# Kernel tuning notes

Measured on AMD Instinct MI355X. Metric: run time of the kernel, lower is better.

Reference implementation:

```python
import jax, jax.numpy as jnp
import numpy as np

B, S, H = 4, 2048, 2048
N_HEADS, KV_HEADS, RANK = 16, 8, 64
HEAD_DIM = H // N_HEADS          # 128
N_REP = N_HEADS // KV_HEADS      # 2
NEG = -1e9


def setup_inputs() -> dict:
    key = jax.random.key(0)
    ks = jax.random.split(key, 6)
    hidden_states = jax.random.normal(ks[0], (B, S, H), dtype=jnp.float32)
    # additive causal mask, broadcast over heads: [B,1,S,S]
    causal = jnp.tril(jnp.ones((S, S), dtype=bool))
    attention_mask = jnp.where(causal, 0.0, NEG).astype(jnp.float32)
    attention_mask = jnp.broadcast_to(attention_mask[None, None], (B, 1, S, S))
    sc = 1.0 / np.sqrt(H)
    Wq = jax.random.normal(ks[1], (H, RANK), dtype=jnp.float32) * sc
    Wk = jax.random.normal(ks[2], (H, RANK), dtype=jnp.float32) * sc
    Wv = jax.random.normal(ks[3], (H, KV_HEADS * HEAD_DIM), dtype=jnp.float32) * sc
    Wo = jax.random.normal(ks[4], (H, H), dtype=jnp.float32) * sc
    return {"hidden_states": hidden_states, "attention_mask": attention_mask,
            "Wq": Wq, "Wk": Wk, "Wv": Wv, "Wo": Wo}


def reference(hidden_states, attention_mask, Wq, Wk, Wv, Wo):
    b, s, h = hidden_states.shape
    # low-rank CP factors shared across heads: [B,S,R]
    q = hidden_states @ Wq
    k = hidden_states @ Wk
    # values with GQA: [B, kv_heads, S, head_dim] -> repeat to [B, n_heads, S, head_dim]
    v = (hidden_states @ Wv).reshape(b, s, KV_HEADS, HEAD_DIM).transpose(0, 2, 1, 3)
    v = jnp.repeat(v, N_REP, axis=1)
    # CP circuit over the (i,j) grid: scores[b,i,j] = sum_r q[b,i,r] * k[b,j,r]
    # (Hadamard over embedding factors gathered at grid indices, SumLayer with unit
    #  weights over rank; the all-ones head factor multiplies by 1). Head-shared.
    scores = jnp.einsum('bir,bjr->bij', q, k)[:, None]  # [B,1,S,S]
    scores = scores + attention_mask                     # additive causal mask
    probs = jax.nn.softmax(scores.astype(jnp.float32), axis=-1).astype(v.dtype)
    # attn_probs @ V, broadcasting the head-shared probs over heads
    ctx = jnp.einsum('bij,bhjd->bhid', probs[:, 0], v)   # [B,H,S,D]
    ctx = ctx.transpose(0, 2, 1, 3).reshape(b, s, h)
    return ctx @ Wo
```

## Files before the change

kernel.cpp:

```cpp
#include <hip/hip_runtime.h>

#define B_ 4
#define S_ 2048
#define H_ 2048
#define R_ 64
#define DKV_ 1024

typedef __attribute__((ext_vector_type(8))) short s16x8;
typedef __attribute__((ext_vector_type(4))) float f32x4v;

__device__ __forceinline__ unsigned short f2bf(float x) {
  unsigned int u = __builtin_bit_cast(unsigned int, x);
  u += 0x7FFF + ((u >> 16) & 1);
  return (unsigned short)(u >> 16);
}
__device__ __forceinline__ float bf2f(unsigned short h) {
  unsigned int u = ((unsigned int)h) << 16;
  return __builtin_bit_cast(float, u);
}

__device__ __forceinline__ void gl_lds16(const void* g, void* l) {
  __builtin_amdgcn_global_load_lds(
      (const __attribute__((address_space(1))) unsigned int*)g,
      (__attribute__((address_space(3))) unsigned int*)l, 16, 0, 0);
}

__device__ __forceinline__ int swz_off(int m, int kb) {
  int L = m >> 1;
  int slot = ((m & 1) << 2) | (kb >> 4);
  int sp = slot ^ (L & 7);
  return (L << 7) | (sp << 4) | (kb & 15);
}

__global__ __launch_bounds__(256) void k_f32_to_bf16x2(const float* __restrict__ in,
    unsigned short* __restrict__ hi, unsigned short* __restrict__ lo, int n4) {
  int i = blockIdx.x * 256 + threadIdx.x;
  if (i >= n4) return;
  float4 v = ((const float4*)in)[i];
  ushort4 h, l;
  h.x = f2bf(v.x); h.y = f2bf(v.y); h.z = f2bf(v.z); h.w = f2bf(v.w);
  l.x = f2bf(v.x - bf2f(h.x)); l.y = f2bf(v.y - bf2f(h.y));
  l.z = f2bf(v.z - bf2f(h.z)); l.w = f2bf(v.w - bf2f(h.w));
  ((ushort4*)hi)[i] = h;
  ((ushort4*)lo)[i] = l;
}

__global__ __launch_bounds__(256) void k_transpose_bf16(const float* __restrict__ in,
    unsigned short* __restrict__ out, int rows, int cols) {
  __shared__ float tile[32][33];
  int c0 = blockIdx.x * 32, r0 = blockIdx.y * 32;
  int tx = threadIdx.x & 31, ty = threadIdx.x >> 5;
  for (int i = 0; i < 4; ++i)
    tile[ty + i * 8][tx] = in[(size_t)(r0 + ty + i * 8) * cols + c0 + tx];
  __syncthreads();
  for (int i = 0; i < 4; ++i)
    out[(size_t)(c0 + ty + i * 8) * rows + r0 + tx] = f2bf(tile[tx][ty + i * 8]);
}

__global__ __launch_bounds__(256) void k_build_wqkt(const float* __restrict__ Wq,
    const float* __restrict__ Wk, unsigned short* __restrict__ hiT,
    unsigned short* __restrict__ loT) {
  __shared__ float tile[32][33];
  int k0 = blockIdx.x * 32, n0 = blockIdx.y * 32;
  const float* W = (n0 < 64) ? Wq : Wk;
  int nb = n0 & 63;
  int tx = threadIdx.x & 31, ty = threadIdx.x >> 5;
  for (int i = 0; i < 4; ++i)
    tile[ty + i * 8][tx] = W[(size_t)(k0 + ty + i * 8) * R_ + nb + tx];
  __syncthreads();
  for (int i = 0; i < 4; ++i) {
    float v = tile[tx][ty + i * 8];
    unsigned short h = f2bf(v);
    size_t idx = (size_t)(n0 + ty + i * 8) * H_ + k0 + tx;
    hiT[idx] = h;
    loT[idx] = f2bf(v - bf2f(h));
  }
}

__global__ __launch_bounds__(256) void k_build_wot(const float* __restrict__ Wo,
                                                   unsigned short* __restrict__ WoT) {
  __shared__ float tile[32][33];
  int n0 = blockIdx.x * 32, r0 = blockIdx.y * 32;
  int h1b = 256 * (r0 >> 7) + (r0 & 127);
  int tx = threadIdx.x & 31, ty = threadIdx.x >> 5;
  for (int i = 0; i < 4; ++i) {
    int dr = ty + i * 8;
    tile[dr][tx] = Wo[(size_t)(h1b + dr) * H_ + n0 + tx] +
                   Wo[(size_t)(h1b + 128 + dr) * H_ + n0 + tx];
  }
  __syncthreads();
  for (int i = 0; i < 4; ++i)
    WoT[(size_t)(n0 + ty + i * 8) * DKV_ + r0 + tx] = f2bf(tile[tx][ty + i * 8]);
}

__global__ __launch_bounds__(256) void k_qk_mfma(
    const unsigned short* __restrict__ Ahi, const unsigned short* __restrict__ Alo,
    const unsigned short* __restrict__ Bhi, const unsigned short* __restrict__ Blo,
    unsigned short* __restrict__ qkh, unsigned short* __restrict__ qkl) {
  constexpr int TQK = 20480;
  __shared__ __attribute__((aligned(16))) char lds[3 * TQK];
  int m0 = blockIdx.x * 32;
  int t = threadIdx.x;
  int lane = t & 63, wave = t >> 6;
  int lr = lane & 15, kb = (lane >> 4) << 4;

  auto stage = [&](int kt, int buf) {
    int k0 = kt << 5;
    char* base = &lds[buf * TQK];
    {
      int q = t & 127;
      int L = q >> 3;
      int slot = (q & 7) ^ (L & 7);
      int m = (L << 1) | (slot >> 2);
      int ke = (slot & 3) << 3;
      const unsigned short* src =
          (t < 128 ? Ahi : Alo) + (size_t)(m0 + m) * H_ + k0 + ke;
      gl_lds16(src, base + (t < 128 ? 0 : 2048) + q * 16);
    }
#pragma unroll
    for (int c = 0; c < 2; ++c) {
      int q = c * 256 + t;
      int L = q >> 3;
      int slot = (q & 7) ^ (L & 7);
      int n = (L << 1) | (slot >> 2);
      int ke = (slot & 3) << 3;
      gl_lds16(Bhi + (size_t)n * H_ + k0 + ke, base + 4096 + q * 16);
    }
#pragma unroll
    for (int c = 0; c < 2; ++c) {
      int q = c * 256 + t;
      int L = q >> 3;
      int slot = (q & 7) ^ (L & 7);
      int n = (L << 1) | (slot >> 2);
      int ke = (slot & 3) << 3;
      gl_lds16(Blo + (size_t)n * H_ + k0 + ke, base + 12288 + q * 16);
    }
  };

  f32x4v acc[2][2] = {};
  stage(0, 0);
  stage(1, 1);
  int cur = 0, nxt = 2;
  for (int kt = 0; kt < 64; ++kt) {
    __builtin_amdgcn_sched_barrier(0);
    if (kt < 63) asm volatile("s_waitcnt vmcnt(5)" ::: "memory");
    else asm volatile("s_waitcnt vmcnt(0)" ::: "memory");
    __builtin_amdgcn_s_barrier();
    __builtin_amdgcn_sched_barrier(0);
    if (kt + 2 < 64) stage(kt + 2, nxt);
    const char* base = &lds[cur * TQK];
    s16x8 ah[2], al[2], bh[2], bl[2];
#pragma unroll
    for (int m = 0; m < 2; ++m) {
      int o = swz_off(m * 16 + lr, kb);
      ah[m] = *(const s16x8*)(base + o);
      al[m] = *(const s16x8*)(base + 2048 + o);
    }
#pragma unroll
    for (int n = 0; n < 2; ++n) {
      int o = swz_off(wave * 32 + n * 16 + lr, kb);
      bh[n] = *(const s16x8*)(base + 4096 + o);
      bl[n] = *(const s16x8*)(base + 12288 + o);
    }
    __builtin_amdgcn_s_setprio(1);
#pragma unroll
    for (int m = 0; m < 2; ++m)
#pragma unroll
      for (int n = 0; n < 2; ++n) {
        acc[m][n] = __builtin_amdgcn_mfma_f32_16x16x32_bf16(ah[m], bh[n], acc[m][n], 0, 0, 0);
        acc[m][n] = __builtin_amdgcn_mfma_f32_16x16x32_bf16(ah[m], bl[n], acc[m][n], 0, 0, 0);
        acc[m][n] = __builtin_amdgcn_mfma_f32_16x16x32_bf16(al[m], bh[n], acc[m][n], 0, 0, 0);
      }
    __builtin_amdgcn_s_setprio(0);
    cur = (cur == 2) ? 0 : cur + 1;
    nxt = (nxt == 2) ? 0 : nxt + 1;
  }
  for (int m = 0; m < 2; ++m) {
    int lrow = m * 16 + ((lane >> 4) << 2);
    for (int n = 0; n < 2; ++n) {
      int lcol = wave * 32 + n * 16 + lr;
      for (int r = 0; r < 4; ++r) {
        float v = acc[m][n][r];
        unsigned short h = f2bf(v);
        size_t idx = (size_t)(m0 + lrow + r) * 128 + lcol;
        qkh[idx] = h;
        qkl[idx] = f2bf(v - bf2f(h));
      }
    }
  }
}

__global__ __launch_bounds__(256) void k_scores_mfma(
    const unsigned short* __restrict__ qkh, const unsigned short* __restrict__ qkl,
    unsigned short* __restrict__ probs, float* __restrict__ part) {
  __shared__ unsigned short AsH[128 * 32], AsL[128 * 32];
  __shared__ unsigned short BsH[128 * 32], BsL[128 * 32];
  __shared__ float psum[128];
  int tri = blockIdx.x, b = blockIdx.y;
  int t = threadIdx.x;
  int it = (int)((sqrtf(8.f * tri + 1.f) - 1.f) * 0.5f);
  while ((it + 1) * (it + 2) / 2 <= tri) ++it;
  while (it * (it + 1) / 2 > tri) --it;
  int jt = tri - it * (it + 1) / 2;
  int i0 = it * 128, j0 = jt * 128;
  const unsigned short* Ah = qkh + (size_t)(b * S_ + i0) * 128;
  const unsigned short* Al = qkl + (size_t)(b * S_ + i0) * 128;
  const unsigned short* Bh = qkh + (size_t)(b * S_ + j0) * 128 + 64;
  const unsigned short* Bl = qkl + (size_t)(b * S_ + j0) * 128 + 64;
  if (t < 128) psum[t] = 0.f;
  int lane = t & 63, wave = t >> 6;
  int wr = wave >> 1, wc = wave & 1;
  int lr = lane & 15, lk = (lane >> 4) * 8;
  f32x4v acc[4][4] = {};
  for (int k0 = 0; k0 < 64; k0 += 32) {
    for (int c = 0; c < 2; ++c) {
      int id = c * 256 + t;
      int row = id >> 2, kc = (id & 3) * 8;
      gl_lds16(Ah + (size_t)row * 128 + k0 + kc, &AsH[row * 32 + kc]);
      gl_lds16(Al + (size_t)row * 128 + k0 + kc, &AsL[row * 32 + kc]);
      gl_lds16(Bh + (size_t)row * 128 + k0 + kc, &BsH[row * 32 + kc]);
      gl_lds16(Bl + (size_t)row * 128 + k0 + kc, &BsL[row * 32 + kc]);
    }
    __syncthreads();
    s16x8 ah[4], al[4], bh[4], bl[4];
    for (int m = 0; m < 4; ++m) {
      ah[m] = *(const s16x8*)&AsH[(wr * 64 + m * 16 + lr) * 32 + lk];
      al[m] = *(const s16x8*)&AsL[(wr * 64 + m * 16 + lr) * 32 + lk];
    }
    for (int n = 0; n < 4; ++n) {
      bh[n] = *(const s16x8*)&BsH[(wc * 64 + n * 16 + lr) * 32 + lk];
      bl[n] = *(const s16x8*)&BsL[(wc * 64 + n * 16 + lr) * 32 + lk];
    }
    for (int m = 0; m < 4; ++m)
      for (int n = 0; n < 4; ++n) {
        acc[m][n] = __builtin_amdgcn_mfma_f32_16x16x32_bf16(ah[m], bh[n], acc[m][n], 0, 0, 0);
        acc[m][n] = __builtin_amdgcn_mfma_f32_16x16x32_bf16(ah[m], bl[n], acc[m][n], 0, 0, 0);
        acc[m][n] = __builtin_amdgcn_mfma_f32_16x16x32_bf16(al[m], bh[n], acc[m][n], 0, 0, 0);
      }
    __syncthreads();
  }
  unsigned short* Pp = probs + (size_t)b * S_ * S_;
  for (int m = 0; m < 4; ++m) {
    int lrow = wr * 64 + m * 16 + ((lane >> 4) << 2);
    float ps[4] = {0.f, 0.f, 0.f, 0.f};
    for (int n = 0; n < 4; ++n) {
      int j = j0 + wc * 64 + n * 16 + lr;
      for (int r = 0; r < 4; ++r) {
        int i = i0 + lrow + r;
        float p = (j <= i) ? __expf(acc[m][n][r]) : 0.f;
        ps[r] += p;
        Pp[(size_t)i * S_ + j] = f2bf(p);
      }
    }
    for (int r = 0; r < 4; ++r) {
      float v = ps[r];
      for (int msk = 1; msk < 16; msk <<= 1) v += __shfl_xor(v, msk, 64);
      if (lr == 0) atomicAdd(&psum[lrow + r], v);
    }
  }
  __syncthreads();
  if (t < 128) part[(size_t)(b * 16 + jt) * S_ + i0 + t] = psum[t];
}

__global__ __launch_bounds__(256) void k_rowsum_recip(const float* __restrict__ part,
                                                      float* __restrict__ recip) {
  int g = blockIdx.x * 256 + threadIdx.x;
  int b = g >> 11, i = g & (S_ - 1);
  int it = i >> 7;
  float s = 0.f;
  for (int jt = 0; jt <= it; ++jt) s += part[(size_t)(b * 16 + jt) * S_ + i];
  recip[(size_t)b * S_ + i] = 1.f / s;
}

template <int BM, int BN, bool TRANS_OUT, bool OUT_BF16, bool SCALE, bool CAUSAL>
__global__ __launch_bounds__(512, 4) void k_gemm256(
    const unsigned short* __restrict__ A, int lda, long batchA,
    const unsigned short* __restrict__ BT, int ldbt, long batchBT,
    void* __restrict__ C, int ldc, long batchC,
    const float* __restrict__ recip, int batchR, int K) {
  constexpr int ABYTES = BM * 64;
  constexpr int BBYTES = BN * 64;
  constexpr int TILEB = ABYTES + BBYTES;
  constexpr int WARPS_M = (BM >= 256) ? 4 : 2;
  constexpr int WARPS_N = 8 / WARPS_M;
  constexpr int WM = BM / WARPS_M;
  constexpr int WN = BN / WARPS_N;
  constexpr int MF = WM / 16;
  constexpr int NF = WN / 16;
  constexpr int LPS = BM / 128 + BN / 128;
  __shared__ __attribute__((aligned(16))) char lds[3 * TILEB];
  __shared__ float s_recip[BM];

  int t = threadIdx.x;
  int gx = gridDim.x;
  int bx, by;
  if (CAUSAL) {
    int x = blockIdx.x;
    bx = (x & 1) ? (gx - 1 - (x >> 1)) : (x >> 1);
    if (blockIdx.z & 2) bx = gx - 1 - bx;
    by = blockIdx.y;
  } else {
    int id = blockIdx.y * gx + blockIdx.x;
    int cpx = gx >> 3;
    int xcd = id & 7, rr = id >> 3;
    bx = xcd * cpx + rr % cpx;
    by = rr / cpx;
  }
  int z = blockIdx.z;
  int m0 = bx * BM, n0 = by * BN;

  const unsigned short* Ab = A + (long)z * batchA + (size_t)m0 * lda;
  const unsigned short* Bb = BT + (long)z * batchBT + (size_t)n0 * ldbt;

  if (SCALE && t < BM) s_recip[t] = recip[(long)z * batchR + m0 + t];

  int lane = t & 63, wave = t >> 6;
  int wr = wave / WARPS_N, wc = wave % WARPS_N;
  int kb = (lane >> 4) << 4;
  int aoff[MF], boff[NF];
#pragma unroll
  for (int mf = 0; mf < MF; ++mf)
    aoff[mf] = swz_off(wr * WM + mf * 16 + (lane & 15), kb);
#pragma unroll
  for (int nf = 0; nf < NF; ++nf)
    boff[nf] = swz_off(wc * WN + nf * 16 + (lane & 15), kb);

  int NT = (CAUSAL ? (m0 + BM) : K) >> 5;

  auto stage = [&](int kt, int buf) {
    int k0 = kt << 5;
    char* la = &lds[buf * TILEB];
    char* lb = la + ABYTES;
#pragma unroll
    for (int c = 0; c < BM / 128; ++c) {
      int q = c * 512 + t;
      int L = q >> 3;
      int slot = (q & 7) ^ (L & 7);
      int m = (L << 1) | (slot >> 2);
      int ke = (slot & 3) << 3;
      gl_lds16(Ab + (size_t)m * lda + k0 + ke, la + q * 16);
    }
#pragma unroll
    for (int c = 0; c < BN / 128; ++c) {
      int q = c * 512 + t;
      int L = q >> 3;
      int slot = (q & 7) ^ (L & 7);
      int n = (L << 1) | (slot >> 2);
      int ke = (slot & 3) << 3;
      gl_lds16(Bb + (size_t)n * ldbt + k0 + ke, lb + q * 16);
    }
  };

  f32x4v acc[MF][NF] = {};
  stage(0, 0);
  if (NT > 1) stage(1, 1);
  int cur = 0, nxt = 2;
  for (int kt = 0; kt < NT; ++kt) {
    __builtin_amdgcn_sched_barrier(0);
    if (kt + 1 < NT) {
      if constexpr (LPS == 2) asm volatile("s_waitcnt vmcnt(2)" ::: "memory");
      else if constexpr (LPS == 3) asm volatile("s_waitcnt vmcnt(3)" ::: "memory");
      else asm volatile("s_waitcnt vmcnt(4)" ::: "memory");
    } else {
      asm volatile("s_waitcnt vmcnt(0)" ::: "memory");
    }
    __builtin_amdgcn_s_barrier();
    __builtin_amdgcn_sched_barrier(0);
    if (kt + 2 < NT) stage(kt + 2, nxt);
    const char* la = &lds[cur * TILEB];
    const char* lb = la + ABYTES;
    s16x8 af[MF], bf[NF];
#pragma unroll
    for (int mf = 0; mf < MF; ++mf) af[mf] = *(const s16x8*)(la + aoff[mf]);
#pragma unroll
    for (int nf = 0; nf < NF; ++nf) bf[nf] = *(const s16x8*)(lb + boff[nf]);
    __builtin_amdgcn_s_setprio(1);
#pragma unroll
    for (int mf = 0; mf < MF; ++mf)
#pragma unroll
      for (int nf = 0; nf < NF; ++nf)
        acc[mf][nf] =
            __builtin_amdgcn_mfma_f32_16x16x32_bf16(af[mf], bf[nf], acc[mf][nf], 0, 0, 0);
    __builtin_amdgcn_s_setprio(0);
    cur = (cur == 2) ? 0 : cur + 1;
    nxt = (nxt == 2) ? 0 : nxt + 1;
  }

#pragma unroll
  for (int mf = 0; mf < MF; ++mf) {
    int lrow = wr * WM + mf * 16 + ((lane >> 4) << 2);
#pragma unroll
    for (int nf = 0; nf < NF; ++nf) {
      int lcol = wc * WN + nf * 16 + (lane & 15);
      f32x4v v = acc[mf][nf];
      if (TRANS_OUT) {
        float f0 = v[0], f1 = v[1], f2 = v[2], f3 = v[3];
        if (SCALE) {
          f0 *= s_recip[lrow]; f1 *= s_recip[lrow + 1];
          f2 *= s_recip[lrow + 2]; f3 *= s_recip[lrow + 3];
        }
        ushort4 o;
        o.x = f2bf(f0); o.y = f2bf(f1); o.z = f2bf(f2); o.w = f2bf(f3);
        unsigned short* Cp = (unsigned short*)C + (long)z * batchC;
        *(ushort4*)&Cp[(size_t)(n0 + lcol) * ldc + m0 + lrow] = o;
      } else {
#pragma unroll
        for (int r = 0; r < 4; ++r) {
          float f = v[r];
          if (SCALE) f *= s_recip[lrow + r];
          if (OUT_BF16) {
            unsigned short* Cp = (unsigned short*)C + (long)z * batchC;
            Cp[(size_t)(m0 + lrow + r) * ldc + n0 + lcol] = f2bf(f);
          } else {
            float* Cp = (float*)C + (long)z * batchC;
            Cp[(size_t)(m0 + lrow + r) * ldc + n0 + lcol] = f;
          }
        }
      }
    }
  }
}

extern "C" void kernel_launch(void* const* d_in, const int* in_sizes, int n_in,
                              void* d_out, int out_size, void* d_ws, size_t ws_size,
                              hipStream_t stream) {
  const float* hs = (const float*)d_in[0];
  const float* Wq = (const float*)d_in[2];
  const float* Wk = (const float*)d_in[3];
  const float* Wv = (const float*)d_in[4];
  const float* Wo = (const float*)d_in[5];
  float* out = (float*)d_out;

  char* w = (char*)d_ws;
  unsigned short* hsb = (unsigned short*)w; w += (size_t)B_ * S_ * H_ * 2;
  unsigned short* hsl = (unsigned short*)w; w += (size_t)B_ * S_ * H_ * 2;
  unsigned short* WvT = (unsigned short*)w; w += (size_t)DKV_ * H_ * 2;
  unsigned short* WoT = (unsigned short*)w; w += (size_t)H_ * DKV_ * 2;
  unsigned short* WqkTh = (unsigned short*)w; w += (size_t)128 * H_ * 2;
  unsigned short* WqkTl = (unsigned short*)w; w += (size_t)128 * H_ * 2;
  unsigned short* VT  = (unsigned short*)w; w += (size_t)DKV_ * B_ * S_ * 2;
  unsigned short* probs = (unsigned short*)w; w += (size_t)B_ * S_ * S_ * 2;
  unsigned short* ctx = (unsigned short*)w; w += (size_t)B_ * S_ * DKV_ * 2;
  unsigned short* qkh = (unsigned short*)w; w += (size_t)B_ * S_ * 128 * 2;
  unsigned short* qkl = (unsigned short*)w; w += (size_t)B_ * S_ * 128 * 2;
  float* part = (float*)w; w += (size_t)B_ * 16 * S_ * 4;
  float* recip = (float*)w; w += (size_t)B_ * S_ * 4;

  k_f32_to_bf16x2<<<(B_ * S_ * H_ / 4 + 255) / 256, 256, 0, stream>>>(
      hs, hsb, hsl, B_ * S_ * H_ / 4);
  k_transpose_bf16<<<dim3(DKV_ / 32, H_ / 32), 256, 0, stream>>>(Wv, WvT, H_, DKV_);
  k_build_wot<<<dim3(H_ / 32, DKV_ / 32), 256, 0, stream>>>(Wo, WoT);
  k_build_wqkt<<<dim3(H_ / 32, 4), 256, 0, stream>>>(Wq, Wk, WqkTh, WqkTl);
  k_qk_mfma<<<B_ * S_ / 32, 256, 0, stream>>>(hsb, hsl, WqkTh, WqkTl, qkh, qkl);
  k_gemm256<256, 128, true, true, false, false>
      <<<dim3(B_ * S_ / 256, DKV_ / 128, 1), 512, 0, stream>>>(
      hsb, H_, 0, WvT, H_, 0, VT, B_ * S_, 0, nullptr, 0, H_);
  k_scores_mfma<<<dim3(136, B_), 256, 0, stream>>>(qkh, qkl, probs, part);
  k_rowsum_recip<<<B_ * S_ / 256, 256, 0, stream>>>(part, recip);
  k_gemm256<128, 128, false, true, true, true>
      <<<dim3(S_ / 128, DKV_ / 128, B_), 512, 0, stream>>>(
      probs, S_, (long)S_ * S_, VT, B_ * S_, S_, ctx, DKV_, (long)S_ * DKV_, recip, S_, S_);
  k_gemm256<256, 128, false, false, false, false>
      <<<dim3(B_ * S_ / 256, H_ / 128, 1), 512, 0, stream>>>(
      ctx, DKV_, 0, WoT, DKV_, 0, out, H_, 0, nullptr, 0, DKV_);
}
```

Baseline: 211.0 us.

## Split GEMM k-loop into two half-MFMA phases interleaved with staged loads

Splits each k-iteration of the bf16 GEMM into two phases. Each phase loads half the A fragments from LDS, issues either the A or the B global-to-LDS prefetch for tile kt+2, then runs half the MFMAs, with extra barriers and lgkmcnt waits between phases. The aim is to spread the memory issue across the compute and interleave LDS reads with MFMA work, in the style of a ping-pong schedule. The vmcnt wait is also changed to 3 for the LPS==4 configuration. The cost is two more workgroup barriers per iteration. The vmcnt accounting is a risk because the loads are now issued in split order.

New measurement: 211.5 us. No clear change (+0.2%).

```diff
diff --git a/kernel.cpp b/kernel.cpp
--- a/kernel.cpp
+++ b/kernel.cpp
@@ -287,6 +287,7 @@
   constexpr int WN = BN / WARPS_N;
   constexpr int MF = WM / 16;
   constexpr int NF = WN / 16;
+  constexpr int MH = MF / 2;
   constexpr int LPS = BM / 128 + BN / 128;
   __shared__ __attribute__((aligned(16))) char lds[3 * TILEB];
   __shared__ float s_recip[BM];
@@ -327,10 +328,9 @@
 
   int NT = (CAUSAL ? (m0 + BM) : K) >> 5;
 
-  auto stage = [&](int kt, int buf) {
+  auto stageA = [&](int kt, int buf) {
     int k0 = kt << 5;
     char* la = &lds[buf * TILEB];
-    char* lb = la + ABYTES;
 #pragma unroll
     for (int c = 0; c < BM / 128; ++c) {
       int q = c * 512 + t;
@@ -340,6 +340,10 @@
       int ke = (slot & 3) << 3;
       gl_lds16(Ab + (size_t)m * lda + k0 + ke, la + q * 16);
     }
+  };
+  auto stageB = [&](int kt, int buf) {
+    int k0 = kt << 5;
+    char* lb = &lds[buf * TILEB] + ABYTES;
 #pragma unroll
     for (int c = 0; c < BN / 128; ++c) {
       int q = c * 512 + t;
@@ -352,36 +356,56 @@
   };
 
   f32x4v acc[MF][NF] = {};
-  stage(0, 0);
-  if (NT > 1) stage(1, 1);
+  stageA(0, 0); stageB(0, 0);
+  if (NT > 1) { stageA(1, 1); stageB(1, 1); }
   int cur = 0, nxt = 2;
   for (int kt = 0; kt < NT; ++kt) {
     __builtin_amdgcn_sched_barrier(0);
     if (kt + 1 < NT) {
       if constexpr (LPS == 2) asm volatile("s_waitcnt vmcnt(2)" ::: "memory");
-      else if constexpr (LPS == 3) asm volatile("s_waitcnt vmcnt(3)" ::: "memory");
-      else asm volatile("s_waitcnt vmcnt(4)" ::: "memory");
+      else asm volatile("s_waitcnt vmcnt(3)" ::: "memory");
     } else {
       asm volatile("s_waitcnt vmcnt(0)" ::: "memory");
     }
     __builtin_amdgcn_s_barrier();
     __builtin_amdgcn_sched_barrier(0);
-    if (kt + 2 < NT) stage(kt + 2, nxt);
     const char* la = &lds[cur * TILEB];
     const char* lb = la + ABYTES;
-    s16x8 af[MF], bf[NF];
-#pragma unroll
-    for (int mf = 0; mf < MF; ++mf) af[mf] = *(const s16x8*)(la + aoff[mf]);
-#pragma unroll
-    for (int nf = 0; nf < NF; ++nf) bf[nf] = *(const s16x8*)(lb + boff[nf]);
+    s16x8 af0[MH], bfv[NF], af1[MH];
+#pragma unroll
+    for (int mf = 0; mf < MH; ++mf) af0[mf] = *(const s16x8*)(la + aoff[mf]);
+#pragma unroll
+    for (int nf = 0; nf < NF; ++nf) bfv[nf] = *(const s16x8*)(lb + boff[nf]);
+    if (kt + 2 < NT) stageA(kt + 2, nxt);
+    __builtin_amdgcn_sched_barrier(0);
+    __builtin_amdgcn_s_barrier();
+    asm volatile("s_waitcnt lgkmcnt(0)" ::: "memory");
+    __builtin_amdgcn_sched_barrier(0);
     __builtin_amdgcn_s_setprio(1);
 #pragma unroll
-    for (int mf = 0; mf < MF; ++mf)
+    for (int mf = 0; mf < MH; ++mf)
 #pragma unroll
       for (int nf = 0; nf < NF; ++nf)
         acc[mf][nf] =
-            __builtin_amdgcn_mfma_f32_16x16x32_bf16(af[mf], bf[nf], acc[mf][nf], 0, 0, 0);
+            __builtin_amdgcn_mfma_f32_16x16x32_bf16(af0[mf], bfv[nf], acc[mf][nf], 0, 0, 0);
     __builtin_amdgcn_s_setprio(0);
+    __builtin_amdgcn_sched_barrier(0);
+#pragma unroll
+    for (int mf = 0; mf < MH; ++mf) af1[mf] = *(const s16x8*)(la + aoff[MH + mf]);
+    if (kt + 2 < NT) stageB(kt + 2, nxt);
+    __builtin_amdgcn_sched_barrier(0);
+    __builtin_amdgcn_s_barrier();
+    asm volatile("s_waitcnt lgkmcnt(0)" ::: "memory");
+    __builtin_amdgcn_sched_barrier(0);
+    __builtin_amdgcn_s_setprio(1);
+#pragma unroll
+    for (int mf = 0; mf < MH; ++mf)
+#pragma unroll
+      for (int nf = 0; nf < NF; ++nf)
+        acc[MH + mf][nf] =
+            __builtin_amdgcn_mfma_f32_16x16x32_bf16(af1[mf], bfv[nf], acc[MH + mf][nf], 0, 0, 0);
+    __builtin_amdgcn_s_setprio(0);
+    __builtin_amdgcn_sched_barrier(0);
     cur = (cur == 2) ? 0 : cur + 1;
     nxt = (nxt == 2) ? 0 : nxt + 1;
   }
```

## Fuse causal scores, exp, rowsum and P@V into one attention kernel

Applied to the files above, without the earlier changes.

Replaces the separate scores kernel (which wrote a full bf16 probability matrix to global memory), the rowsum reciprocal kernel and the batched causal P@V GEMM with one fused kernel. Each block takes 64 query rows by 256 value columns, computes scores for each 32-key chunk in registers, exponentiates and masks them, stores P in LDS, and runs the P@V MFMAs. The row sums are normalised at the end. This removes the 32MB-scale probs write and read and two launches. In exchange, each d-column block recomputes the scores (4x redundant QK work), the tiles are smaller and there are two barriers per k-step.

After: 201.8 us. 4.4% less time.

```diff
diff --git a/kernel.cpp b/kernel.cpp
--- a/kernel.cpp
+++ b/kernel.cpp
@@ -190,129 +190,189 @@
   }
 }
 
-__global__ __launch_bounds__(256) void k_scores_mfma(
+__global__ __launch_bounds__(512, 4) void k_attn_fused(
     const unsigned short* __restrict__ qkh, const unsigned short* __restrict__ qkl,
-    unsigned short* __restrict__ probs, float* __restrict__ part) {
-  __shared__ unsigned short AsH[128 * 32], AsL[128 * 32];
-  __shared__ unsigned short BsH[128 * 32], BsL[128 * 32];
-  __shared__ float psum[128];
-  int tri = blockIdx.x, b = blockIdx.y;
+    const unsigned short* __restrict__ VT, unsigned short* __restrict__ ctx) {
+  constexpr int TILEB = 24576;
+  __shared__ __attribute__((aligned(16))) char lds[3 * TILEB + 4096 + 256];
+  char* Pt = &lds[3 * TILEB];
+  float* rs = (float*)&lds[3 * TILEB + 4096];
+
   int t = threadIdx.x;
-  int it = (int)((sqrtf(8.f * tri + 1.f) - 1.f) * 0.5f);
-  while ((it + 1) * (it + 2) / 2 <= tri) ++it;
-  while (it * (it + 1) / 2 > tri) --it;
-  int jt = tri - it * (it + 1) / 2;
-  int i0 = it * 128, j0 = jt * 128;
-  const unsigned short* Ah = qkh + (size_t)(b * S_ + i0) * 128;
-  const unsigned short* Al = qkl + (size_t)(b * S_ + i0) * 128;
-  const unsigned short* Bh = qkh + (size_t)(b * S_ + j0) * 128 + 64;
-  const unsigned short* Bl = qkl + (size_t)(b * S_ + j0) * 128 + 64;
-  if (t < 128) psum[t] = 0.f;
+  int gx = gridDim.x;
+  int x = blockIdx.x;
+  int bx = (x & 1) ? (gx - 1 - (x >> 1)) : (x >> 1);
+  if (blockIdx.z & 2) bx = gx - 1 - bx;
+  int z = blockIdx.z;
+  int m0 = bx * 64, d0 = blockIdx.y * 256;
+
   int lane = t & 63, wave = t >> 6;
-  int wr = wave >> 1, wc = wave & 1;
-  int lr = lane & 15, lk = (lane >> 4) * 8;
-  f32x4v acc[4][4] = {};
-  for (int k0 = 0; k0 < 64; k0 += 32) {
+  int sm = wave >> 1, sn = wave & 1;
+  int wr = wave >> 2, wc = wave & 3;
+  int kb = (lane >> 4) << 4;
+
+  const unsigned short* qh = qkh + (size_t)z * S_ * 128;
+  const unsigned short* ql = qkl + (size_t)z * S_ * 128;
+
+  s16x8 qfh[2], qfl[2];
+  {
+    size_t rq = (size_t)(m0 + sm * 16 + (lane & 15)) * 128 + ((lane >> 4) << 3);
+    qfh[0] = *(const s16x8*)(qh + rq);
+    qfh[1] = *(const s16x8*)(qh + rq + 32);
+    qfl[0] = *(const s16x8*)(ql + rq);
+    qfl[1] = *(const s16x8*)(ql + rq + 32);
+  }
+
+  auto stage = [&](int kt, int buf) {
+    int j0 = kt << 5;
+    char* base = &lds[buf * TILEB];
+    {
+      int q = t & 127;
+      int L = q >> 3;
+      int slot = (q & 7) ^ (L & 7);
+      int jr = (L << 1) | (slot >> 2);
+      int ke = (slot & 3) << 3;
+      int sub = t >> 7;
+      const unsigned short* src = ((sub < 2) ? qh : ql) +
+          (size_t)(j0 + jr) * 128 + 64 + ((sub & 1) << 5) + ke;
+      gl_lds16(src, base + sub * 2048 + q * 16);
+    }
+    char* vb = base + 8192;
+#pragma unroll
     for (int c = 0; c < 2; ++c) {
-      int id = c * 256 + t;
-      int row = id >> 2, kc = (id & 3) * 8;
-      gl_lds16(Ah + (size_t)row * 128 + k0 + kc, &AsH[row * 32 + kc]);
-      gl_lds16(Al + (size_t)row * 128 + k0 + kc, &AsL[row * 32 + kc]);
-      gl_lds16(Bh + (size_t)row * 128 + k0 + kc, &BsH[row * 32 + kc]);
-      gl_lds16(Bl + (size_t)row * 128 + k0 + kc, &BsL[row * 32 + kc]);
-    }
-    __syncthreads();
-    s16x8 ah[4], al[4], bh[4], bl[4];
-    for (int m = 0; m < 4; ++m) {
-      ah[m] = *(const s16x8*)&AsH[(wr * 64 + m * 16 + lr) * 32 + lk];
-      al[m] = *(const s16x8*)&AsL[(wr * 64 + m * 16 + lr) * 32 + lk];
-    }
-    for (int n = 0; n < 4; ++n) {
-      bh[n] = *(const s16x8*)&BsH[(wc * 64 + n * 16 + lr) * 32 + lk];
-      bl[n] = *(const s16x8*)&BsL[(wc * 64 + n * 16 + lr) * 32 + lk];
-    }
-    for (int m = 0; m < 4; ++m)
-      for (int n = 0; n < 4; ++n) {
-        acc[m][n] = __builtin_amdgcn_mfma_f32_16x16x32_bf16(ah[m], bh[n], acc[m][n], 0, 0, 0);
-        acc[m][n] = __builtin_amdgcn_mfma_f32_16x16x32_bf16(ah[m], bl[n], acc[m][n], 0, 0, 0);
-        acc[m][n] = __builtin_amdgcn_mfma_f32_16x16x32_bf16(al[m], bh[n], acc[m][n], 0, 0, 0);
+      int q = c * 512 + t;
+      int L = q >> 3;
+      int slot = (q & 7) ^ (L & 7);
+      int dr = (L << 1) | (slot >> 2);
+      int ke = (slot & 3) << 3;
+      gl_lds16(VT + (size_t)(d0 + dr) * (B_ * S_) + (size_t)z * S_ + j0 + ke,
+               vb + q * 16);
+    }
+  };
+
+  if (t < 64) rs[t] = 0.f;
+  int NT = (m0 + 64) >> 5;
+  stage(0, 0);
+  stage(1, 1);
+
+  int jrow = sn * 16 + (lane & 15);
+  int koffs = swz_off(jrow, kb);
+  int paoff[2], voff[4];
+#pragma unroll
+  for (int mf = 0; mf < 2; ++mf)
+    paoff[mf] = swz_off(wr * 32 + mf * 16 + (lane & 15), kb);
+#pragma unroll
+  for (int nf = 0; nf < 4; ++nf)
+    voff[nf] = swz_off(wc * 64 + nf * 16 + (lane & 15), kb);
+
+  float ps[4] = {0.f, 0.f, 0.f, 0.f};
+  f32x4v accp[2][4] = {};
+  int prow = sm * 16 + ((lane >> 4) << 2);
+  int pcol = sn * 16 + (lane & 15);
+
+  int cur = 0, nxt = 2;
+  for (int kt = 0; kt < NT; ++kt) {
+    __builtin_amdgcn_sched_barrier(0);
+    if (kt + 1 < NT) asm volatile("s_waitcnt vmcnt(3) lgkmcnt(0)" ::: "memory");
+    else asm volatile("s_waitcnt vmcnt(0) lgkmcnt(0)" ::: "memory");
+    __builtin_amdgcn_s_barrier();
+    __builtin_amdgcn_sched_barrier(0);
+    if (kt + 2 < NT) stage(kt + 2, nxt);
+    const char* base = &lds[cur * TILEB];
+    s16x8 kh[2], kl[2];
+    kh[0] = *(const s16x8*)(base + koffs);
+    kh[1] = *(const s16x8*)(base + 2048 + koffs);
+    kl[0] = *(const s16x8*)(base + 4096 + koffs);
+    kl[1] = *(const s16x8*)(base + 6144 + koffs);
+    f32x4v s = {};
+#pragma unroll
+    for (int ks = 0; ks < 2; ++ks) {
+      s = __builtin_amdgcn_mfma_f32_16x16x32_bf16(qfh[ks], kh[ks], s, 0, 0, 0);
+      s = __builtin_amdgcn_mfma_f32_16x16x32_bf16(qfh[ks], kl[ks], s, 0, 0, 0);
+      s = __builtin_amdgcn_mfma_f32_16x16x32_bf16(qfl[ks], kh[ks], s, 0, 0, 0);
+    }
+    int jg = (kt << 5) + pcol;
+    int ig = m0 + prow;
+#pragma unroll
+    for (int r = 0; r < 4; ++r) {
+      float p = (jg <= ig + r) ? __expf(s[r]) : 0.f;
+      ps[r] += p;
+      *(unsigned short*)(Pt + swz_off(prow + r, pcol * 2)) = f2bf(p);
+    }
+    __builtin_amdgcn_sched_barrier(0);
+    asm volatile("s_waitcnt lgkmcnt(0)" ::: "memory");
+    __builtin_amdgcn_s_barrier();
+    __builtin_amdgcn_sched_barrier(0);
+    s16x8 pa[2], vf[4];
+#pragma unroll
+    for (int mf = 0; mf < 2; ++mf) pa[mf] = *(const s16x8*)(Pt + paoff[mf]);
+    const char* vbase = base + 8192;
+#pragma unroll
+    for (int nf = 0; nf < 4; ++nf) vf[nf] = *(const s16x8*)(vbase + voff[nf]);
+    __builtin_amdgcn_s_setprio(1);
+#pragma unroll
+    for (int mf = 0; mf < 2; ++mf)
+#pragma unroll
+      for (int nf = 0; nf < 4; ++nf)
+        accp[mf][nf] =
+            __builtin_amdgcn_mfma_f32_16x16x32_bf16(pa[mf], vf[nf], accp[mf][nf], 0, 0, 0);
+    __builtin_amdgcn_s_setprio(0);
+    cur = (cur == 2) ? 0 : cur + 1;
+    nxt = (nxt == 2) ? 0 : nxt + 1;
+  }
+
+#pragma unroll
+  for (int r = 0; r < 4; ++r) {
+    float v = ps[r];
+    for (int msk = 1; msk < 16; msk <<= 1) v += __shfl_xor(v, msk, 64);
+    if ((lane & 15) == 0) atomicAdd(&rs[prow + r], v);
+  }
+  __syncthreads();
+
+  unsigned short* Cp = ctx + (size_t)(z * S_ + m0) * DKV_ + d0;
+#pragma unroll
+  for (int mf = 0; mf < 2; ++mf) {
+    int lr0 = wr * 32 + mf * 16 + ((lane >> 4) << 2);
+#pragma unroll
+    for (int nf = 0; nf < 4; ++nf) {
+      int lc = wc * 64 + nf * 16 + (lane & 15);
+#pragma unroll
+      for (int r = 0; r < 4; ++r) {
+        float sc = 1.f / rs[lr0 + r];
+        Cp[(size_t)(lr0 + r) * DKV_ + lc] = f2bf(accp[mf][nf][r] * sc);
       }
-    __syncthreads();
-  }
-  unsigned short* Pp = probs + (size_t)b * S_ * S_;
-  for (int m = 0; m < 4; ++m) {
-    int lrow = wr * 64 + m * 16 + ((lane >> 4) << 2);
-    float ps[4] = {0.f, 0.f, 0.f, 0.f};
-    for (int n = 0; n < 4; ++n) {
-      int j = j0 + wc * 64 + n * 16 + lr;
-      for (int r = 0; r < 4; ++r) {
-        int i = i0 + lrow + r;
-        float p = (j <= i) ? __expf(acc[m][n][r]) : 0.f;
-        ps[r] += p;
-        Pp[(size_t)i * S_ + j] = f2bf(p);
-      }
-    }
-    for (int r = 0; r < 4; ++r) {
-      float v = ps[r];
-      for (int msk = 1; msk < 16; msk <<= 1) v += __shfl_xor(v, msk, 64);
-      if (lr == 0) atomicAdd(&psum[lrow + r], v);
-    }
-  }
-  __syncthreads();
-  if (t < 128) part[(size_t)(b * 16 + jt) * S_ + i0 + t] = psum[t];
-}
-
-__global__ __launch_bounds__(256) void k_rowsum_recip(const float* __restrict__ part,
-                                                      float* __restrict__ recip) {
-  int g = blockIdx.x * 256 + threadIdx.x;
-  int b = g >> 11, i = g & (S_ - 1);
-  int it = i >> 7;
-  float s = 0.f;
-  for (int jt = 0; jt <= it; ++jt) s += part[(size_t)(b * 16 + jt) * S_ + i];
-  recip[(size_t)b * S_ + i] = 1.f / s;
-}
-
-template <int BM, int BN, bool TRANS_OUT, bool OUT_BF16, bool SCALE, bool CAUSAL>
+    }
+  }
+}
+
+template <int BM, int BN, bool TRANS_OUT, bool OUT_BF16>
 __global__ __launch_bounds__(512, 4) void k_gemm256(
-    const unsigned short* __restrict__ A, int lda, long batchA,
-    const unsigned short* __restrict__ BT, int ldbt, long batchBT,
-    void* __restrict__ C, int ldc, long batchC,
-    const float* __restrict__ recip, int batchR, int K) {
+    const unsigned short* __restrict__ A, int lda,
+    const unsigned short* __restrict__ BT, int ldbt,
+    void* __restrict__ C, int ldc, int K) {
   constexpr int ABYTES = BM * 64;
   constexpr int BBYTES = BN * 64;
   constexpr int TILEB = ABYTES + BBYTES;
-  constexpr int WARPS_M = (BM >= 256) ? 4 : 2;
-  constexpr int WARPS_N = 8 / WARPS_M;
+  constexpr int WARPS_M = 4;
+  constexpr int WARPS_N = 2;
   constexpr int WM = BM / WARPS_M;
   constexpr int WN = BN / WARPS_N;
   constexpr int MF = WM / 16;
   constexpr int NF = WN / 16;
   constexpr int LPS = BM / 128 + BN / 128;
   __shared__ __attribute__((aligned(16))) char lds[3 * TILEB];
-  __shared__ float s_recip[BM];
 
   int t = threadIdx.x;
   int gx = gridDim.x;
-  int bx, by;
-  if (CAUSAL) {
-    int x = blockIdx.x;
-    bx = (x & 1) ? (gx - 1 - (x >> 1)) : (x >> 1);
-    if (blockIdx.z & 2) bx = gx - 1 - bx;
-    by = blockIdx.y;
-  } else {
-    int id = blockIdx.y * gx + blockIdx.x;
-    int cpx = gx >> 3;
-    int xcd = id & 7, rr = id >> 3;
-    bx = xcd * cpx + rr % cpx;
-    by = rr / cpx;
-  }
-  int z = blockIdx.z;
+  int id = blockIdx.y * gx + blockIdx.x;
+  int cpx = gx >> 3;
+  int xcd = id & 7, rr = id >> 3;
+  int bx = xcd * cpx + rr % cpx;
+  int by = rr / cpx;
   int m0 = bx * BM, n0 = by * BN;
 
-  const unsigned short* Ab = A + (long)z * batchA + (size_t)m0 * lda;
-  const unsigned short* Bb = BT + (long)z * batchBT + (size_t)n0 * ldbt;
-
-  if (SCALE && t < BM) s_recip[t] = recip[(long)z * batchR + m0 + t];
+  const unsigned short* Ab = A + (size_t)m0 * lda;
+  const unsigned short* Bb = BT + (size_t)n0 * ldbt;
 
   int lane = t & 63, wave = t >> 6;
   int wr = wave / WARPS_N, wc = wave % WARPS_N;
@@ -325,7 +385,7 @@
   for (int nf = 0; nf < NF; ++nf)
     boff[nf] = swz_off(wc * WN + nf * 16 + (lane & 15), kb);
 
-  int NT = (CAUSAL ? (m0 + BM) : K) >> 5;
+  int NT = K >> 5;
 
   auto stage = [&](int kt, int buf) {
     int k0 = kt << 5;
@@ -359,8 +419,7 @@
     __builtin_amdgcn_sched_barrier(0);
     if (kt + 1 < NT) {
       if constexpr (LPS == 2) asm volatile("s_waitcnt vmcnt(2)" ::: "memory");
-      else if constexpr (LPS == 3) asm volatile("s_waitcnt vmcnt(3)" ::: "memory");
-      else asm volatile("s_waitcnt vmcnt(4)" ::: "memory");
+      else asm volatile("s_waitcnt vmcnt(3)" ::: "memory");
     } else {
       asm volatile("s_waitcnt vmcnt(0)" ::: "memory");
     }
@@ -394,26 +453,19 @@
       int lcol = wc * WN + nf * 16 + (lane & 15);
       f32x4v v = acc[mf][nf];
       if (TRANS_OUT) {
-        float f0 = v[0], f1 = v[1], f2 = v[2], f3 = v[3];
-        if (SCALE) {
-          f0 *= s_recip[lrow]; f1 *= s_recip[lrow + 1];
-          f2 *= s_recip[lrow + 2]; f3 *= s_recip[lrow + 3];
-        }
         ushort4 o;
-        o.x = f2bf(f0); o.y = f2bf(f1); o.z = f2bf(f2); o.w = f2bf(f3);
-        unsigned short* Cp = (unsigned short*)C + (long)z * batchC;
+        o.x = f2bf(v[0]); o.y = f2bf(v[1]); o.z = f2bf(v[2]); o.w = f2bf(v[3]);
+        unsigned short* Cp = (unsigned short*)C;
         *(ushort4*)&Cp[(size_t)(n0 + lcol) * ldc + m0 + lrow] = o;
       } else {
 #pragma unroll
         for (int r = 0; r < 4; ++r) {
-          float f = v[r];
-          if (SCALE) f *= s_recip[lrow + r];
           if (OUT_BF16) {
-            unsigned short* Cp = (unsigned short*)C + (long)z * batchC;
-            Cp[(size_t)(m0 + lrow + r) * ldc + n0 + lcol] = f2bf(f);
+            unsigned short* Cp = (unsigned short*)C;
+            Cp[(size_t)(m0 + lrow + r) * ldc + n0 + lcol] = f2bf(v[r]);
           } else {
-            float* Cp = (float*)C + (long)z * batchC;
-            Cp[(size_t)(m0 + lrow + r) * ldc + n0 + lcol] = f;
+            float* Cp = (float*)C;
+            Cp[(size_t)(m0 + lrow + r) * ldc + n0 + lcol] = v[r];
           }
         }
       }
@@ -439,12 +491,9 @@
   unsigned short* WqkTh = (unsigned short*)w; w += (size_t)128 * H_ * 2;
   unsigned short* WqkTl = (unsigned short*)w; w += (size_t)128 * H_ * 2;
   unsigned short* VT  = (unsigned short*)w; w += (size_t)DKV_ * B_ * S_ * 2;
-  unsigned short* probs = (unsigned short*)w; w += (size_t)B_ * S_ * S_ * 2;
   unsigned short* ctx = (unsigned short*)w; w += (size_t)B_ * S_ * DKV_ * 2;
   unsigned short* qkh = (unsigned short*)w; w += (size_t)B_ * S_ * 128 * 2;
   unsigned short* qkl = (unsigned short*)w; w += (size_t)B_ * S_ * 128 * 2;
-  float* part = (float*)w; w += (size_t)B_ * 16 * S_ * 4;
-  float* recip = (float*)w; w += (size_t)B_ * S_ * 4;
 
   k_f32_to_bf16x2<<<(B_ * S_ * H_ / 4 + 255) / 256, 256, 0, stream>>>(
       hs, hsb, hsl, B_ * S_ * H_ / 4);
@@ -452,15 +501,11 @@
   k_build_wot<<<dim3(H_ / 32, DKV_ / 32), 256, 0, stream>>>(Wo, WoT);
   k_build_wqkt<<<dim3(H_ / 32, 4), 256, 0, stream>>>(Wq, Wk, WqkTh, WqkTl);
   k_qk_mfma<<<B_ * S_ / 32, 256, 0, stream>>>(hsb, hsl, WqkTh, WqkTl, qkh, qkl);
-  k_gemm256<256, 128, true, true, false, false>
-      <<<dim3(B_ * S_ / 256, DKV_ / 128, 1), 512, 0, stream>>>(
-      hsb, H_, 0, WvT, H_, 0, VT, B_ * S_, 0, nullptr, 0, H_);
-  k_scores_mfma<<<dim3(136, B_), 256, 0, stream>>>(qkh, qkl, probs, part);
-  k_rowsum_recip<<<B_ * S_ / 256, 256, 0, stream>>>(part, recip);
-  k_gemm256<128, 128, false, true, true, true>
-      <<<dim3(S_ / 128, DKV_ / 128, B_), 512, 0, stream>>>(
-      probs, S_, (long)S_ * S_, VT, B_ * S_, S_, ctx, DKV_, (long)S_ * DKV_, recip, S_, S_);
-  k_gemm256<256, 128, false, false, false, false>
-      <<<dim3(B_ * S_ / 256, H_ / 128, 1), 512, 0, stream>>>(
-      ctx, DKV_, 0, WoT, DKV_, 0, out, H_, 0, nullptr, 0, DKV_);
-}
+  k_gemm256<256, 128, true, true>
+      <<<dim3(B_ * S_ / 256, DKV_ / 128), 512, 0, stream>>>(
+      hsb, H_, WvT, H_, VT, B_ * S_, H_);
+  k_attn_fused<<<dim3(32, 4, B_), 512, 0, stream>>>(qkh, qkl, VT, ctx);
+  k_gemm256<256, 128, false, false>
+      <<<dim3(B_ * S_ / 256, H_ / 128), 512, 0, stream>>>(
+      ctx, DKV_, WoT, DKV_, out, H_, DKV_);
+}
```
